# Optimization experiments

Hardware: AMD Instinct MI355X
Metric: run time of the kernel (lower is better)

## Reference

```python
import jax, jax.numpy as jnp
import numpy as np

EPS = 1e-5
NUM_GROUPS = 32
N_HEADS = 8


def layer_norm(x, g, b):
    mu = jnp.mean(x, axis=-1, keepdims=True)
    var = jnp.var(x, axis=-1, keepdims=True)
    return (x - mu) * jax.lax.rsqrt(var + EPS) * g + b


def group_norm(x, g, b):
    # x: [B, C, H, W]
    B, C, H, W = x.shape
    xg = x.reshape(B, NUM_GROUPS, C // NUM_GROUPS, H, W)
    mu = jnp.mean(xg, axis=(2, 3, 4), keepdims=True)
    var = jnp.var(xg, axis=(2, 3, 4), keepdims=True)
    xn = ((xg - mu) * jax.lax.rsqrt(var + EPS)).reshape(B, C, H, W)
    return xn * g[None, :, None, None] + b[None, :, None, None]


def attention(x, ctx, wq, wk, wv, wo, bo):
    # x: [B, N, D], ctx: [B, M, Dc]
    B, N, _ = x.shape
    q = x @ wq
    k = ctx @ wk
    v = ctx @ wv
    D = q.shape[-1]
    d = D // N_HEADS
    q = q.reshape(B, N, N_HEADS, d)
    k = k.reshape(B, -1, N_HEADS, d)
    v = v.reshape(B, -1, N_HEADS, d)
    sim = jnp.einsum('bihd,bjhd->bhij', q, k) * (d ** -0.5)
    attn = jax.nn.softmax(sim, axis=-1)
    out = jnp.einsum('bhij,bjhd->bihd', attn, v).reshape(B, N, D)
    return out @ wo + bo


def reference(x, context, gn_g, gn_b, proj_in_w, proj_in_b,
              ln1_g, ln1_b, q1_w, k1_w, v1_w, o1_w, o1_b,
              ln2_g, ln2_b, q2_w, k2_w, v2_w, o2_w, o2_b,
              ln3_g, ln3_b, ff1_w, ff1_b, ff2_w, ff2_b,
              proj_out_w, proj_out_b):
    B, C, H, W = x.shape
    x_in = x
    h = group_norm(x, gn_g, gn_b)
    # 1x1 conv == channel matmul
    h = jnp.einsum('bchw,cd->bhwd', h, proj_in_w) + proj_in_b
    h = h.reshape(B, H * W, -1)  # [B, N, D]
    # BasicTransformerBlock (depth=1)
    h = attention(layer_norm(h, ln1_g, ln1_b), layer_norm(h, ln1_g, ln1_b),
                  q1_w, k1_w, v1_w, o1_w, o1_b) + h
    h = attention(layer_norm(h, ln2_g, ln2_b), context,
                  q2_w, k2_w, v2_w, o2_w, o2_b) + h
    hn = layer_norm(h, ln3_g, ln3_b)
    ff = jax.nn.gelu(hn @ ff1_w + ff1_b, approximate=False) @ ff2_w + ff2_b
    h = ff + h
    h = h.reshape(B, H, W, -1)
    out = jnp.einsum('bhwd,dc->bchw', h, proj_out_w) + proj_out_b[None, :, None, None]
    return out + x_in


def setup_inputs() -> dict:
    key = jax.random.key(0)
    ks = jax.random.split(key, 16)
    B, C, H, W = 8, 512, 32, 32
    D, Dc, L = 512, 768, 77
    s = 0.02

    def rn(k, shape):
        return jax.random.normal(k, shape, jnp.float32) * s

    return dict(
        x=jax.random.normal(ks[0], (B, C, H, W), jnp.float32),
        context=jax.random.normal(ks[1], (B, L, Dc), jnp.float32),
        gn_g=jnp.ones(C, jnp.float32), gn_b=jnp.zeros(C, jnp.float32),
        proj_in_w=rn(ks[2], (C, D)), proj_in_b=jnp.zeros(D, jnp.float32),
        ln1_g=jnp.ones(D, jnp.float32), ln1_b=jnp.zeros(D, jnp.float32),
        q1_w=rn(ks[3], (D, D)), k1_w=rn(ks[4], (D, D)), v1_w=rn(ks[5], (D, D)),
        o1_w=rn(ks[6], (D, D)), o1_b=jnp.zeros(D, jnp.float32),
        ln2_g=jnp.ones(D, jnp.float32), ln2_b=jnp.zeros(D, jnp.float32),
        q2_w=rn(ks[7], (D, D)), k2_w=rn(ks[8], (Dc, D)), v2_w=rn(ks[9], (Dc, D)),
        o2_w=rn(ks[10], (D, D)), o2_b=jnp.zeros(D, jnp.float32),
        ln3_g=jnp.ones(D, jnp.float32), ln3_b=jnp.zeros(D, jnp.float32),
        ff1_w=rn(ks[11], (D, 4 * D)), ff1_b=jnp.zeros(4 * D, jnp.float32),
        ff2_w=rn(ks[12], (4 * D, D)), ff2_b=jnp.zeros(D, jnp.float32),
        proj_out_w=rn(ks[13], (D, C)), proj_out_b=jnp.zeros(C, jnp.float32),
    )
```

## Files before the change

kernel.cpp:

```cpp
#include <hip/hip_runtime.h>

typedef unsigned short u16;
typedef unsigned int   u32;
typedef __bf16 bf16x8 __attribute__((ext_vector_type(8)));
typedef float  f32x4  __attribute__((ext_vector_type(4)));
typedef u16    u16x4  __attribute__((ext_vector_type(4)));

__device__ __forceinline__ float bf2f(u16 u) {
    union { u32 i; float f; } v; v.i = (u32)u << 16; return v.f;
}
__device__ __forceinline__ u16 f2bf(float f) {
    union { float f; u32 u; } v; v.f = f;
    u32 r = v.u + 0x7fffu + ((v.u >> 16) & 1u);
    return (u16)(r >> 16);
}
__device__ __forceinline__ float ldn(const void* p, size_t i, u32 f) {
    return f ? bf2f(((const u16*)p)[i]) : ((const float*)p)[i];
}
__device__ __forceinline__ u32 dtf(const void* gref) {
    return (((const u32*)gref)[0] == 0x3F803F80u) ? 1u : 0u;
}
__device__ __forceinline__ void async16(const void* g, void* l) {
    __builtin_amdgcn_global_load_lds(
        (__attribute__((address_space(1))) u32*)g,
        (__attribute__((address_space(3))) u32*)l, 16, 0, 0);
}
__device__ __forceinline__ float fast_erf(float x) {
    float ax = fabsf(x);
    float t = __frcp_rn(1.f + 0.3275911f * ax);
    float p = t * (0.254829592f + t * (-0.284496736f + t * (1.421413741f +
              t * (-1.453152027f + t * 1.061405429f))));
    float r = 1.f - p * __expf(-ax * ax);
    return copysignf(r, x);
}

struct TrTab {
    const void* in[12];
    u16* out[12];
    int K[12]; int N[12]; int blk0[13];
};

__global__ __launch_bounds__(256)
void prep_k(TrTab tab, int trN,
            const void* __restrict__ ctx, u16* __restrict__ ctxb, int cvtB,
            const void* __restrict__ X, const void* __restrict__ G,
            const void* __restrict__ Bt, u16* __restrict__ gout)
{
    const u32 f = dtf(G);
    const int blk = blockIdx.x;
    const int t = threadIdx.x;

    if (blk < 256) {
        __shared__ float gtile[16][264];
        __shared__ float red[8];
        __shared__ float gsh[16], bsh[16];
        const int b = blk >> 5, g = blk & 31;
        const int c0 = g * 16;
        const size_t xbase = ((size_t)b * 512 + c0) * 1024;
        if (t < 16) { gsh[t] = ldn(G, c0 + t, f); bsh[t] = ldn(Bt, c0 + t, f); }
        float s = 0.f, sq = 0.f;
        if (f) {
            for (int i = 0; i < 8; ++i) {
                union { uint4 v; u16 u[8]; } ld;
                ld.v = *(const uint4*)((const u16*)X + xbase + i * 2048 + t * 8);
#pragma unroll
                for (int j = 0; j < 8; ++j) { float v = bf2f(ld.u[j]); s += v; sq += v * v; }
            }
        } else {
            for (int i = 0; i < 16; ++i) {
                float4 v4 = *(const float4*)((const float*)X + xbase + i * 1024 + t * 4);
                s += v4.x + v4.y + v4.z + v4.w;
                sq += v4.x * v4.x + v4.y * v4.y + v4.z * v4.z + v4.w * v4.w;
            }
        }
        for (int off = 32; off; off >>= 1) { s += __shfl_xor(s, off); sq += __shfl_xor(sq, off); }
        const int w = t >> 6, lane = t & 63;
        if (lane == 0) { red[w] = s; red[4 + w] = sq; }
        __syncthreads();
        s  = red[0] + red[1] + red[2] + red[3];
        sq = red[4] + red[5] + red[6] + red[7];
        const float mean = s * (1.f / 16384.f);
        const float rstd = rsqrtf(sq * (1.f / 16384.f) - mean * mean + 1e-5f);
        for (int ch = 0; ch < 4; ++ch) {
            const int hw0 = ch * 256;
            __syncthreads();
#pragma unroll
            for (int k = 0; k < 4; ++k) {
                int slot = k * 256 + t;
                int row = slot >> 6, col = (slot & 63) * 4;
                float4 v4;
                if (f) {
                    union { uint2 v; u16 u[4]; } ld;
                    ld.v = *(const uint2*)((const u16*)X + xbase + (size_t)row * 1024 + hw0 + col);
                    v4.x = bf2f(ld.u[0]); v4.y = bf2f(ld.u[1]);
                    v4.z = bf2f(ld.u[2]); v4.w = bf2f(ld.u[3]);
                } else {
                    v4 = *(const float4*)((const float*)X + xbase + (size_t)row * 1024 + hw0 + col);
                }
                *(float4*)(&gtile[row][col]) = v4;
            }
            __syncthreads();
#pragma unroll
            for (int k = 0; k < 2; ++k) {
                int slot = k * 256 + t;
                int hwl = slot >> 1, ci0 = (slot & 1) * 8;
                union { uint4 v; u16 u[8]; } st;
#pragma unroll
                for (int j = 0; j < 8; ++j) {
                    float v = gtile[ci0 + j][hwl];
                    st.u[j] = f2bf((v - mean) * rstd * gsh[ci0 + j] + bsh[ci0 + j]);
                }
                *(uint4*)(&gout[((size_t)b * 1024 + hw0 + hwl) * 512 + c0 + ci0]) = st.v;
            }
        }
        return;
    }
    const int blk2 = blk - 256;
    if (blk2 < trN) {
        __shared__ u16 tile[32][33];
        int i = 0;
        while (i < 11 && blk2 >= tab.blk0[i + 1]) ++i;
        const void* In = tab.in[i];
        u16* Out = tab.out[i];
        const int K = tab.K[i], N = tab.N[i];
        const int lb = blk2 - tab.blk0[i];
        const int nx = N >> 5;
        const int n0 = (lb % nx) * 32, k0 = (lb / nx) * 32;
        const int tx = t & 31, ty = t >> 5;
#pragma unroll
        for (int s = 0; s < 32; s += 8)
            tile[ty + s][tx] = f2bf(ldn(In, (size_t)(k0 + ty + s) * N + n0 + tx, f));
        __syncthreads();
#pragma unroll
        for (int s = 0; s < 32; s += 8)
            Out[(size_t)(n0 + ty + s) * K + k0 + tx] = tile[tx][ty + s];
        return;
    }
    {
        int i = ((blk2 - trN) * 256 + t) * 8;
        union { uint4 v; u16 u[8]; } st;
#pragma unroll
        for (int j = 0; j < 8; ++j) st.u[j] = f2bf(ldn(ctx, i + j, f));
        *(uint4*)(&ctxb[i]) = st.v;
    }
}

__global__ __launch_bounds__(256)
void ln_k(const u16* __restrict__ X, const void* __restrict__ G,
          const void* __restrict__ Bt, u16* __restrict__ Out,
          const void* __restrict__ fref)
{
    const u32 f = dtf(fref);
    const int t = threadIdx.x, w = t >> 6, lane = t & 63;
    const size_t row = (size_t)blockIdx.x * 4 + w;
    const int col0 = lane * 8;
    union { uint4 v; u16 u[8]; } ld, st;
    ld.v = *(const uint4*)(&X[row * 512 + col0]);
    float fv[8]; float s = 0.f, sq = 0.f;
#pragma unroll
    for (int j = 0; j < 8; ++j) { fv[j] = bf2f(ld.u[j]); s += fv[j]; sq += fv[j] * fv[j]; }
    for (int off = 32; off; off >>= 1) { s += __shfl_xor(s, off); sq += __shfl_xor(sq, off); }
    const float mean = s * (1.f / 512.f);
    const float rstd = rsqrtf(sq * (1.f / 512.f) - mean * mean + 1e-5f);
#pragma unroll
    for (int j = 0; j < 8; ++j)
        st.u[j] = f2bf((fv[j] - mean) * rstd * ldn(G, col0 + j, f) + ldn(Bt, col0 + j, f));
    *(uint4*)(&Out[row * 512 + col0]) = st.v;
}

template<int MODE, int BM, int BN, int BK>
__global__ __launch_bounds__(256, (BM == 64) ? 4 : 2)
void gemm_k(const u16* __restrict__ A, const u16* __restrict__ Wt,
            const void* __restrict__ bias, const u16* Res,
            const void* __restrict__ Xres, void* Out, u16* __restrict__ Pv,
            int M, int N, int K, int MT, int NT, const void* __restrict__ fref)
{
    const u32 f = dtf(fref);
    constexpr int MI = BM / 32;
    constexpr int NI = BN / 32;
    constexpr int KC = BK / 32;
    constexpr int CPR = BK / 8;
    constexpr int SA = (BM * BK) / 2048;
    constexpr int SB = (BN * BK) / 2048;
    __shared__ u16 As[2][BM * BK];
    __shared__ u16 Bs[2][BN * BK];
    const int t = threadIdx.x;
    const int lane = t & 63;
    const int l15 = lane & 15;
    const int quad = lane >> 4;
    const int w = t >> 6;
    const int rowbase = (w >> 1) * (BM / 2);
    const int colbase = (w & 1) * (BN / 2);

    int m_t, n_t;
    {
        const int id = blockIdx.x;
        if ((MT & 7) == 0) {
            const int low = id & 7, k = id >> 3;
            n_t = k % NT;
            m_t = ((k / NT) << 3) | low;
        } else {
            n_t = id % NT;
            m_t = id / NT;
        }
    }
    const int m0 = m_t * BM;
    const int n0 = n_t * BN;

    const int nkt = K / BK;

    auto stage = [&](int kt, int buf) {
        const int k0 = kt * BK;
#pragma unroll
        for (int s = 0; s < SA; ++s) {
            int c = t + s * 256;
            int r = c / CPR, ch = c % CPR;
            int gch = (BK == 32) ? (ch ^ ((r >> 1) & 3)) : (ch ^ (r & 7));
            int gr = m0 + r; gr = gr < M ? gr : M - 1;
            async16(A + (size_t)gr * K + k0 + gch * 8, (char*)&As[buf][0] + (size_t)c * 16);
        }
#pragma unroll
        for (int s = 0; s < SB; ++s) {
            int c = t + s * 256;
            int r = c / CPR, ch = c % CPR;
            int gch = (BK == 32) ? (ch ^ ((r >> 1) & 3)) : (ch ^ (r & 7));
            async16(Wt + (size_t)(n0 + r) * K + k0 + gch * 8, (char*)&Bs[buf][0] + (size_t)c * 16);
        }
    };

    f32x4 acc[MI][NI];
#pragma unroll
    for (int i = 0; i < MI; ++i)
#pragma unroll
        for (int j = 0; j < NI; ++j)
#pragma unroll
            for (int e = 0; e < 4; ++e) acc[i][j][e] = 0.f;

    const int swz = (BK == 32) ? ((l15 >> 1) & 3) : (l15 & 7);

    stage(0, 0);
    for (int kt = 0; kt < nkt; ++kt) {
        const int buf = kt & 1;
        __syncthreads();
        if (kt + 1 < nkt) stage(kt + 1, buf ^ 1);

        bf16x8 af[MI][KC], bfr[NI][KC];
#pragma unroll
        for (int ks = 0; ks < KC; ++ks) {
#pragma unroll
            for (int mi = 0; mi < MI; ++mi)
                af[mi][ks] = *(const bf16x8*)(&As[buf][(rowbase + mi * 16 + l15) * BK + (((quad + 4 * ks) ^ swz) * 8)]);
#pragma unroll
            for (int ni = 0; ni < NI; ++ni)
                bfr[ni][ks] = *(const bf16x8*)(&Bs[buf][(colbase + ni * 16 + l15) * BK + (((quad + 4 * ks) ^ swz) * 8)]);
        }
#pragma unroll
        for (int ks = 0; ks < KC; ++ks)
#pragma unroll
            for (int mi = 0; mi < MI; ++mi)
#pragma unroll
                for (int ni = 0; ni < NI; ++ni)
                    acc[mi][ni] = __builtin_amdgcn_mfma_f32_16x16x32_bf16(af[mi][ks], bfr[ni][ks], acc[mi][ni], 0, 0, 0);
    }

#pragma unroll
    for (int mi = 0; mi < MI; ++mi) {
#pragma unroll
        for (int ni = 0; ni < NI; ++ni) {
            const int col = n0 + colbase + ni * 16 + l15;
            float bv = 0.f;
            if (MODE == 0 || MODE == 1 || MODE == 2)
                bv = bias ? ldn(bias, col, f) : 0.f;
            const int row0 = m0 + rowbase + mi * 16 + quad * 4;

            if (MODE == 2) {
                size_t o0 = ((size_t)(row0 >> 10) * 512 + col) * 1024 + (row0 & 1023);
                if (f) {
                    u16x4 st;
#pragma unroll
                    for (int r = 0; r < 4; ++r)
                        st[r] = f2bf(acc[mi][ni][r] + bv + bf2f(((const u16*)Xres)[o0 + r]));
                    *(u16x4*)((u16*)Out + o0) = st;
                } else {
                    float4 xr = *(const float4*)((const float*)Xres + o0);
                    float4 st;
                    st.x = acc[mi][ni][0] + bv + xr.x;
                    st.y = acc[mi][ni][1] + bv + xr.y;
                    st.z = acc[mi][ni][2] + bv + xr.z;
                    st.w = acc[mi][ni][3] + bv + xr.w;
                    *(float4*)((float*)Out + o0) = st;
                }
                continue;
            }
            if (MODE == 3 && col >= 1024) {
                size_t o0 = ((size_t)(row0 >> 10) * 512 + (col - 1024)) * 1024 + (row0 & 1023);
                u16x4 st;
#pragma unroll
                for (int r = 0; r < 4; ++r) st[r] = f2bf(acc[mi][ni][r]);
                *(u16x4*)(Pv + o0) = st;
                continue;
            }

#pragma unroll
            for (int r = 0; r < 4; ++r) {
                const int row = row0 + r;
                if (row >= M) continue;
                float v = acc[mi][ni][r] + bv;
                if (MODE == 1) v = 0.5f * v * (1.f + fast_erf(v * 0.70710678118654752f));
                if (MODE == 3) {
                    ((u16*)Out)[(size_t)(col >> 9) * (8192 * 512) + (size_t)row * 512 + (col & 511)] = f2bf(v);
                } else if (MODE == 4) {
                    if (col < 512) {
                        ((u16*)Out)[(size_t)row * 512 + col] = f2bf(v);
                    } else {
                        u32 b = ((u32)row * 54472u) >> 22;
                        u32 j = (u32)row - b * 77u;
                        Pv[((size_t)b * 512 + (col - 512)) * 128 + j] = f2bf(v);
                    }
                } else {
                    size_t oidx = (size_t)row * N + col;
                    if (Res) v += bf2f(Res[oidx]);
                    ((u16*)Out)[oidx] = f2bf(v);
                }
            }
        }
    }
}

template<int VS>
__global__ __launch_bounds__(256, 2)
void attn_k(const u16* __restrict__ Q, const u16* __restrict__ Kb,
            const u16* __restrict__ VbT, u16* __restrict__ O, int MK)
{
    __shared__ u16 Ks[64 * 72];
    __shared__ u16 Vts[64 * 72];
    __shared__ u16 Ps[4][16 * 72];
    const int t = threadIdx.x, lane = t & 63, w = t >> 6;
    const int l15 = lane & 15, quad = lane >> 4;
    const int bh = blockIdx.y, b = bh >> 3, h = bh & 7;
    const int q0 = blockIdx.x * 64, hc0 = h * 64;
    const size_t qrow0 = (size_t)b * 1024 + q0;
    const size_t kvbase = (size_t)b * MK;
    const size_t vtbase = ((size_t)b * 512 + hc0) * VS;
    const float SC = 0.18033688011112042f;

    bf16x8 aq[2];
#pragma unroll
    for (int ks = 0; ks < 2; ++ks)
        aq[ks] = *(const bf16x8*)(&Q[(qrow0 + w * 16 + l15) * 512 + hc0 + ks * 32 + quad * 8]);

    float lsum[4] = {0.f, 0.f, 0.f, 0.f};
    f32x4 o_acc[4];
#pragma unroll
    for (int ni = 0; ni < 4; ++ni)
#pragma unroll
        for (int e = 0; e < 4; ++e) o_acc[ni][e] = 0.f;

    const int nkt = (MK + 63) >> 6;
    for (int kt = 0; kt < nkt; ++kt) {
        __syncthreads();
#pragma unroll
        for (int s = 0; s < 2; ++s) {
            int c = t + s * 256; int r = c >> 3, d0 = (c & 7) * 8;
            int j = kt * 64 + r; j = j < MK ? j : MK - 1;
            *(uint4*)(&Ks[r * 72 + d0]) = *(const uint4*)(&Kb[(kvbase + j) * 512 + hc0 + d0]);
            *(uint4*)(&Vts[r * 72 + d0]) = *(const uint4*)(&VbT[vtbase + (size_t)r * VS + kt * 64 + d0]);
        }
        __syncthreads();

        f32x4 sa[4];
#pragma unroll
        for (int ni = 0; ni < 4; ++ni)
#pragma unroll
            for (int e = 0; e < 4; ++e) sa[ni][e] = 0.f;
#pragma unroll
        for (int ks = 0; ks < 2; ++ks)
#pragma unroll
            for (int ni = 0; ni < 4; ++ni) {
                bf16x8 bk = *(const bf16x8*)(&Ks[(ni * 16 + l15) * 72 + ks * 32 + quad * 8]);
                sa[ni] = __builtin_amdgcn_mfma_f32_16x16x32_bf16(aq[ks], bk, sa[ni], 0, 0, 0);
            }

#pragma unroll
        for (int ni = 0; ni < 4; ++ni) {
            const bool valid = (kt * 64 + ni * 16 + l15) < MK;
#pragma unroll
            for (int r = 0; r < 4; ++r) {
                float sv = valid ? fminf(sa[ni][r] * SC, 60.f) : -1e30f;
                float pv = exp2f(sv);
                lsum[r] += pv;
                Ps[w][(quad * 4 + r) * 72 + ni * 16 + l15] = f2bf(pv);
            }
        }
#pragma unroll
        for (int ks = 0; ks < 2; ++ks) {
            bf16x8 ap = *(const bf16x8*)(&Ps[w][l15 * 72 + ks * 32 + quad * 8]);
#pragma unroll
            for (int ni = 0; ni < 4; ++ni) {
                bf16x8 bv = *(const bf16x8*)(&Vts[(ni * 16 + l15) * 72 + ks * 32 + quad * 8]);
                o_acc[ni] = __builtin_amdgcn_mfma_f32_16x16x32_bf16(ap, bv, o_acc[ni], 0, 0, 0);
            }
        }
    }
#pragma unroll
    for (int off = 1; off < 16; off <<= 1)
#pragma unroll
        for (int r = 0; r < 4; ++r) lsum[r] += __shfl_xor(lsum[r], off);
    float inv[4];
#pragma unroll
    for (int r = 0; r < 4; ++r) inv[r] = 1.f / fmaxf(lsum[r], 1e-30f);
#pragma unroll
    for (int ni = 0; ni < 4; ++ni)
#pragma unroll
        for (int r = 0; r < 4; ++r) {
            size_t row = qrow0 + w * 16 + quad * 4 + r;
            O[row * 512 + hc0 + ni * 16 + l15] = f2bf(o_acc[ni][r] * inv[r]);
        }
}

extern "C" void kernel_launch(void* const* d_in, const int* in_sizes, int n_in,
                              void* d_out, int out_size, void* d_ws, size_t ws_size,
                              hipStream_t stream)
{
    const void* x    = d_in[0];
    const void* ctx  = d_in[1];
    const void* gn_g = d_in[2];
    const void* gn_b = d_in[3];
    const void* piw  = d_in[4];
    const void* pib  = d_in[5];
    const void* ln1g = d_in[6];
    const void* ln1b = d_in[7];
    const void* q1w  = d_in[8];
    const void* k1w  = d_in[9];
    const void* v1w  = d_in[10];
    const void* o1w  = d_in[11];
    const void* o1b  = d_in[12];
    const void* ln2g = d_in[13];
    const void* ln2b = d_in[14];
    const void* q2w  = d_in[15];
    const void* k2w  = d_in[16];
    const void* v2w  = d_in[17];
    const void* o2w  = d_in[18];
    const void* o2b  = d_in[19];
    const void* ln3g = d_in[20];
    const void* ln3b = d_in[21];
    const void* f1w  = d_in[22];
    const void* f1b  = d_in[23];
    const void* f2w  = d_in[24];
    const void* f2b  = d_in[25];
    const void* pwo  = d_in[26];
    const void* pob  = d_in[27];

    u16* ws = (u16*)d_ws;
    size_t o = 0;
    u16* WT_qkv1 = ws + o; o += (size_t)1536 * 512;
    u16* WT_kv2  = ws + o; o += (size_t)1024 * 768;
    u16* WT_pi = ws + o; o += 512 * 512;
    u16* WT_o1 = ws + o; o += 512 * 512;
    u16* WT_q2 = ws + o; o += 512 * 512;
    u16* WT_o2 = ws + o; o += 512 * 512;
    u16* WT_f1 = ws + o; o += (size_t)2048 * 512;
    u16* WT_f2 = ws + o; o += (size_t)512 * 2048;
    u16* WT_po = ws + o; o += 512 * 512;
    u16* ctxb  = ws + o; o += (size_t)616 * 768;
    u16* vbTc  = ws + o; o += (size_t)8 * 512 * 128;
    u16* hb    = ws + o; o += (size_t)8192 * 512;
    u16* t0    = ws + o; o += (size_t)8192 * 512;
    u16* qb    = ws + o; o += (size_t)8192 * 512;
    u16* kb    = ws + o; o += (size_t)8192 * 512;
    u16* ab    = ws + o; o += (size_t)8192 * 512;
    u16* vbT   = ws + o; o += (size_t)8192 * 512;
    u16* ffm   = qb;

    dim3 tb(256);

    {
        TrTab tab;
        const void* ins[12] = {q1w, k1w, v1w, k2w, v2w, piw, o1w, q2w, o2w, f1w, f2w, pwo};
        u16* outs[12] = {WT_qkv1, WT_qkv1 + (size_t)512 * 512, WT_qkv1 + (size_t)1024 * 512,
                         WT_kv2, WT_kv2 + (size_t)512 * 768,
                         WT_pi, WT_o1, WT_q2, WT_o2, WT_f1, WT_f2, WT_po};
        int Ks[12] = {512, 512, 512, 768, 768, 512, 512, 512, 512, 512, 2048, 512};
        int Ns[12] = {512, 512, 512, 512, 512, 512, 512, 512, 512, 2048, 512, 512};
        int acc0 = 0;
        for (int i = 0; i < 12; ++i) {
            tab.in[i] = ins[i]; tab.out[i] = outs[i]; tab.K[i] = Ks[i]; tab.N[i] = Ns[i];
            tab.blk0[i] = acc0; acc0 += (Ns[i] / 32) * (Ks[i] / 32);
        }
        tab.blk0[12] = acc0;
        const int cvtB = 473088 / (8 * 256);
        prep_k<<<dim3(256 + acc0 + cvtB), tb, 0, stream>>>(
            tab, acc0, ctx, ctxb, cvtB, x, gn_g, gn_b, t0);
    }

    gemm_k<0, 64, 64, 64><<<dim3(1024), tb, 0, stream>>>(t0, WT_pi, pib, nullptr, nullptr, hb, nullptr, 8192, 512, 512, 128, 8, gn_g);

    ln_k<<<dim3(2048), tb, 0, stream>>>(hb, ln1g, ln1b, t0, gn_g);
    gemm_k<3, 64, 64, 64><<<dim3(3072), tb, 0, stream>>>(t0, WT_qkv1, nullptr, nullptr, nullptr, qb, vbT, 8192, 1536, 512, 128, 24, gn_g);
    attn_k<1024><<<dim3(16, 64), tb, 0, stream>>>(qb, kb, vbT, ab, 1024);
    gemm_k<0, 64, 64, 64><<<dim3(1024), tb, 0, stream>>>(ab, WT_o1, o1b, hb, nullptr, hb, nullptr, 8192, 512, 512, 128, 8, gn_g);

    ln_k<<<dim3(2048), tb, 0, stream>>>(hb, ln2g, ln2b, t0, gn_g);
    gemm_k<0, 64, 64, 64><<<dim3(1024), tb, 0, stream>>>(t0, WT_q2, nullptr, nullptr, nullptr, qb, nullptr, 8192, 512, 512, 128, 8, gn_g);
    gemm_k<4, 64, 64, 64><<<dim3(160), tb, 0, stream>>>(ctxb, WT_kv2, nullptr, nullptr, nullptr, kb, vbTc, 616, 1024, 768, 10, 16, gn_g);
    attn_k<128><<<dim3(16, 64), tb, 0, stream>>>(qb, kb, vbTc, ab, 77);
    gemm_k<0, 64, 64, 64><<<dim3(1024), tb, 0, stream>>>(ab, WT_o2, o2b, hb, nullptr, hb, nullptr, 8192, 512, 512, 128, 8, gn_g);

    ln_k<<<dim3(2048), tb, 0, stream>>>(hb, ln3g, ln3b, t0, gn_g);
    gemm_k<1, 64, 64, 64><<<dim3(4096), tb, 0, stream>>>(t0, WT_f1, f1b, nullptr, nullptr, ffm, nullptr, 8192, 2048, 512, 128, 32, gn_g);
    gemm_k<0, 64, 64, 64><<<dim3(1024), tb, 0, stream>>>(ffm, WT_f2, f2b, hb, nullptr, hb, nullptr, 8192, 512, 2048, 128, 8, gn_g);

    gemm_k<2, 64, 64, 64><<<dim3(1024), tb, 0, stream>>>(hb, WT_po, pob, nullptr, x, d_out, nullptr, 8192, 512, 512, 128, 8, gn_g);
}
```

Before: 430.6 us.

## Double-buffer attention K/V tiles with async LDS loads and XOR swizzle

The attention kernel now stages K and V tiles into two LDS buffers using async global-to-LDS loads, so the next tile's fetch overlaps the current tile's MFMA work. This needs only one barrier per iteration instead of two. The padded LDS rows are replaced by an XOR chunk swizzle to avoid bank conflicts, which saves LDS space for the second buffer. The grid becomes one-dimensional with heads in the low bits of the block index, and bounds masking is compiled out for the full-length self-attention case. The gain relies on the barrier making the async loads visible before they are read.

```diff
diff --git a/kernel.cpp b/kernel.cpp
--- a/kernel.cpp
+++ b/kernel.cpp
@@ -332,17 +332,19 @@
 void attn_k(const u16* __restrict__ Q, const u16* __restrict__ Kb,
             const u16* __restrict__ VbT, u16* __restrict__ O, int MK)
 {
-    __shared__ u16 Ks[64 * 72];
-    __shared__ u16 Vts[64 * 72];
+    __shared__ u16 Ks[2][64 * 64];
+    __shared__ u16 Vts[2][64 * 64];
     __shared__ u16 Ps[4][16 * 72];
     const int t = threadIdx.x, lane = t & 63, w = t >> 6;
     const int l15 = lane & 15, quad = lane >> 4;
-    const int bh = blockIdx.y, b = bh >> 3, h = bh & 7;
-    const int q0 = blockIdx.x * 64, hc0 = h * 64;
+    const int id = blockIdx.x;
+    const int bh = id & 63, b = bh >> 3, h = bh & 7;
+    const int q0 = (id >> 6) * 64, hc0 = h * 64;
     const size_t qrow0 = (size_t)b * 1024 + q0;
     const size_t kvbase = (size_t)b * MK;
     const size_t vtbase = ((size_t)b * 512 + hc0) * VS;
     const float SC = 0.18033688011112042f;
+    constexpr bool FULL = (VS == 1024);
 
     bf16x8 aq[2];
 #pragma unroll
@@ -357,16 +359,34 @@
         for (int e = 0; e < 4; ++e) o_acc[ni][e] = 0.f;
 
     const int nkt = (MK + 63) >> 6;
+
+    auto stage = [&](int kt, int buf) {
+#pragma unroll
+        for (int s = 0; s < 2; ++s) {
+            int c = t + s * 256;
+            int r = c >> 3, ch = c & 7;
+            int gch = ch ^ (r & 7);
+            int j = kt * 64 + r; j = j < MK ? j : MK - 1;
+            async16(Kb + (kvbase + j) * 512 + hc0 + gch * 8,
+                    (char*)&Ks[buf][0] + (size_t)c * 16);
+        }
+#pragma unroll
+        for (int s = 0; s < 2; ++s) {
+            int c = t + s * 256;
+            int r = c >> 3, ch = c & 7;
+            int gch = ch ^ (r & 7);
+            async16(VbT + vtbase + (size_t)r * VS + kt * 64 + gch * 8,
+                    (char*)&Vts[buf][0] + (size_t)c * 16);
+        }
+    };
+
+    const int swz = l15 & 7;
+
+    stage(0, 0);
     for (int kt = 0; kt < nkt; ++kt) {
+        const int buf = kt & 1;
         __syncthreads();
-#pragma unroll
-        for (int s = 0; s < 2; ++s) {
-            int c = t + s * 256; int r = c >> 3, d0 = (c & 7) * 8;
-            int j = kt * 64 + r; j = j < MK ? j : MK - 1;
-            *(uint4*)(&Ks[r * 72 + d0]) = *(const uint4*)(&Kb[(kvbase + j) * 512 + hc0 + d0]);
-            *(uint4*)(&Vts[r * 72 + d0]) = *(const uint4*)(&VbT[vtbase + (size_t)r * VS + kt * 64 + d0]);
-        }
-        __syncthreads();
+        if (kt + 1 < nkt) stage(kt + 1, buf ^ 1);
 
         f32x4 sa[4];
 #pragma unroll
@@ -377,13 +397,13 @@
         for (int ks = 0; ks < 2; ++ks)
 #pragma unroll
             for (int ni = 0; ni < 4; ++ni) {
-                bf16x8 bk = *(const bf16x8*)(&Ks[(ni * 16 + l15) * 72 + ks * 32 + quad * 8]);
+                bf16x8 bk = *(const bf16x8*)(&Ks[buf][(ni * 16 + l15) * 64 + (((quad + 4 * ks) ^ swz) * 8)]);
                 sa[ni] = __builtin_amdgcn_mfma_f32_16x16x32_bf16(aq[ks], bk, sa[ni], 0, 0, 0);
             }
 
 #pragma unroll
         for (int ni = 0; ni < 4; ++ni) {
-            const bool valid = (kt * 64 + ni * 16 + l15) < MK;
+            const bool valid = FULL || (kt * 64 + ni * 16 + l15) < MK;
 #pragma unroll
             for (int r = 0; r < 4; ++r) {
                 float sv = valid ? fminf(sa[ni][r] * SC, 60.f) : -1e30f;
@@ -397,7 +417,7 @@
             bf16x8 ap = *(const bf16x8*)(&Ps[w][l15 * 72 + ks * 32 + quad * 8]);
 #pragma unroll
             for (int ni = 0; ni < 4; ++ni) {
-                bf16x8 bv = *(const bf16x8*)(&Vts[(ni * 16 + l15) * 72 + ks * 32 + quad * 8]);
+                bf16x8 bv = *(const bf16x8*)(&Vts[buf][(ni * 16 + l15) * 64 + (((quad + 4 * ks) ^ swz) * 8)]);
                 o_acc[ni] = __builtin_amdgcn_mfma_f32_16x16x32_bf16(ap, bv, o_acc[ni], 0, 0, 0);
             }
         }
@@ -497,13 +517,13 @@
 
     ln_k<<<dim3(2048), tb, 0, stream>>>(hb, ln1g, ln1b, t0, gn_g);
     gemm_k<3, 64, 64, 64><<<dim3(3072), tb, 0, stream>>>(t0, WT_qkv1, nullptr, nullptr, nullptr, qb, vbT, 8192, 1536, 512, 128, 24, gn_g);
-    attn_k<1024><<<dim3(16, 64), tb, 0, stream>>>(qb, kb, vbT, ab, 1024);
+    attn_k<1024><<<dim3(1024), tb, 0, stream>>>(qb, kb, vbT, ab, 1024);
     gemm_k<0, 64, 64, 64><<<dim3(1024), tb, 0, stream>>>(ab, WT_o1, o1b, hb, nullptr, hb, nullptr, 8192, 512, 512, 128, 8, gn_g);
 
     ln_k<<<dim3(2048), tb, 0, stream>>>(hb, ln2g, ln2b, t0, gn_g);
     gemm_k<0, 64, 64, 64><<<dim3(1024), tb, 0, stream>>>(t0, WT_q2, nullptr, nullptr, nullptr, qb, nullptr, 8192, 512, 512, 128, 8, gn_g);
     gemm_k<4, 64, 64, 64><<<dim3(160), tb, 0, stream>>>(ctxb, WT_kv2, nullptr, nullptr, nullptr, kb, vbTc, 616, 1024, 768, 10, 16, gn_g);
-    attn_k<128><<<dim3(16, 64), tb, 0, stream>>>(qb, kb, vbTc, ab, 77);
+    attn_k<128><<<dim3(1024), tb, 0, stream>>>(qb, kb, vbTc, ab, 77);
     gemm_k<0, 64, 64, 64><<<dim3(1024), tb, 0, stream>>>(ab, WT_o2, o2b, hb, nullptr, hb, nullptr, 8192, 512, 512, 128, 8, gn_g);
 
     ln_k<<<dim3(2048), tb, 0, stream>>>(hb, ln3g, ln3b, t0, gn_g);
```

New measurement: 420.3 us. -2.4%, faster.
